# Optimization experiments

Measured on AMD Instinct MI355X. Metric: run time of the kernel, lower is better.

The kernel has to match this reference:

```python
import jax, jax.numpy as jnp
import numpy as np

T, D = 4096, 1536          # tokens, hidden
H, KV, HD = 24, 8, 64      # heads, kv heads, head dim
E, TOPK, F = 32, 8, 512    # experts, top-k, expert intermediate
FS = 1024                  # shared-MLP intermediate
THETA = 10000.0
AMULT = 0.015625           # attention_multiplier (replaces 1/sqrt(hd))
RMULT = 0.22               # residual_multiplier
EPS = 1e-6


def setup_inputs() -> dict:
    key = jax.random.key(0)
    ks = jax.random.split(key, 12)
    s = 0.02
    return {
        'positions': jnp.arange(T, dtype=jnp.int32),
        'hidden_states': jax.random.normal(ks[0], (T, D), jnp.float32),
        'ln1_w': jnp.ones((D,), jnp.float32),
        'wq': jax.random.normal(ks[1], (D, H * HD), jnp.float32) * s,
        'wk': jax.random.normal(ks[2], (D, KV * HD), jnp.float32) * s,
        'wv': jax.random.normal(ks[3], (D, KV * HD), jnp.float32) * s,
        'wo': jax.random.normal(ks[4], (H * HD, D), jnp.float32) * s,
        'ln2_w': jnp.ones((D,), jnp.float32),
        'router_w': jax.random.normal(ks[5], (D, E), jnp.float32) * s,
        'w_gate_up': jax.random.normal(ks[6], (E, D, 2 * F), jnp.float32) * s,
        'w_down': jax.random.normal(ks[7], (E, F, D), jnp.float32) * s,
        'shared_gate_up': jax.random.normal(ks[8], (D, 2 * FS), jnp.float32) * s,
        'shared_down': jax.random.normal(ks[9], (FS, D), jnp.float32) * s,
    }


def _rmsnorm(x, w):
    var = jnp.mean(x * x, axis=-1, keepdims=True)
    return x * jax.lax.rsqrt(var + EPS) * w


def _rope(x, positions):
    # x: [T, nH, HD], neox-style half rotation
    half = HD // 2
    inv_freq = 1.0 / (THETA ** (jnp.arange(half, dtype=jnp.float32) / half))
    ang = positions.astype(jnp.float32)[:, None] * inv_freq[None, :]  # [T, half]
    cos, sin = jnp.cos(ang)[:, None, :], jnp.sin(ang)[:, None, :]
    x1, x2 = x[..., :half], x[..., half:]
    return jnp.concatenate([x1 * cos - x2 * sin, x2 * cos + x1 * sin], axis=-1)


def _silu_and_mul(gu):
    g, u = jnp.split(gu, 2, axis=-1)
    return jax.nn.silu(g) * u


def reference(positions, hidden_states, ln1_w, wq, wk, wv, wo, ln2_w,
              router_w, w_gate_up, w_down, shared_gate_up, shared_down):
    # ---- attention block ----
    residual = hidden_states
    h = _rmsnorm(hidden_states, ln1_w)
    q = _rope((h @ wq).reshape(T, H, HD), positions)
    k = _rope((h @ wk).reshape(T, KV, HD), positions)
    v = (h @ wv).reshape(T, KV, HD)
    k = jnp.repeat(k, H // KV, axis=1)  # GQA expand -> [T, H, HD]
    v = jnp.repeat(v, H // KV, axis=1)
    scores = jnp.einsum('thd,shd->hts', q, k) * AMULT
    mask = jnp.tril(jnp.ones((T, T), dtype=bool))
    scores = jnp.where(mask[None], scores, jnp.finfo(scores.dtype).min)
    probs = jax.nn.softmax(scores, axis=-1)
    attn = jnp.einsum('hts,shd->thd', probs, v).reshape(T, H * HD) @ wo
    hidden = residual + attn * RMULT

    # ---- MoE + shared MLP block ----
    residual = hidden
    h = _rmsnorm(hidden, ln2_w)
    # router: top-k logits, softmax over selected (renormalized gates)
    logits = h @ router_w                          # [T, E]
    topv, topi = jax.lax.top_k(logits, TOPK)       # [T, TOPK]
    gates = jax.nn.softmax(topv, axis=-1)
    # per-token dense expert weight map [T, E] (zero for unselected experts)
    wmap = jnp.sum(jax.nn.one_hot(topi, E, dtype=h.dtype) * gates[..., None], axis=1)
    gu = jnp.einsum('td,edf->tef', h, w_gate_up)   # [T, E, 2F]
    act = _silu_and_mul(gu)                        # [T, E, F]
    moe_out = jnp.einsum('tef,efd,te->td', act, w_down, wmap)
    # shared SiLU MLP
    shared = _silu_and_mul(h @ shared_gate_up) @ shared_down
    hidden = residual + (moe_out + shared) * RMULT
    return hidden
```

## Files before the change

kernel.cpp:

```cpp
#include <hip/hip_runtime.h>
#include <hip/hip_bf16.h>
#include <stdint.h>

using u16 = unsigned short;
using u32 = unsigned int;

typedef __attribute__((ext_vector_type(8))) short short8;
typedef __attribute__((ext_vector_type(4))) short short4v;
typedef __attribute__((ext_vector_type(4))) float f32x4;

#define MFMA16(a,b,c) __builtin_amdgcn_mfma_f32_16x16x32_bf16(a,b,c,0,0,0)
#define QSCL 0.022542110325192448f


__device__ __forceinline__ u16 f2bf(float f){
  __hip_bfloat16 b = __float2bfloat16(f);
  return *reinterpret_cast<u16*>(&b);
}
__device__ __forceinline__ float bf2f(u16 b){ return __uint_as_float(((u32)b)<<16); }

__device__ __forceinline__ void gload16(const void* g, void* l){
  __builtin_amdgcn_global_load_lds(
      (const __attribute__((address_space(1))) u32*)g,
      (__attribute__((address_space(3))) u32*)l, 16, 0, 0);
}

template<int CTRL>
__device__ __forceinline__ float dppf(float x){
  return __int_as_float(__builtin_amdgcn_mov_dpp(__float_as_int(x), CTRL, 0xf, 0xf, true));
}
__device__ __forceinline__ float red16_sum(float x){
  x += dppf<0x128>(x);
  x += dppf<0x124>(x);
  x += dppf<0x122>(x);
  x += dppf<0x121>(x);
  return x;
}

__global__ __launch_bounds__(256) void k_wt(const float* __restrict__ src,
    u16* __restrict__ dst, int K, int N, long sstride, long dstride)
{
  __shared__ float tile[64][65];
  int nb = blockIdx.x*64, kb = blockIdx.y*64;
  const float* S = src + (long)blockIdx.z*sstride;
  u16* D = dst + (long)blockIdx.z*dstride;
  int tid = threadIdx.x;
  int rr = tid>>4, c4 = (tid&15)*4;
  #pragma unroll
  for (int p=0;p<4;++p){
    int r = p*16 + rr;
    f32x4 v = *(const f32x4*)&S[(long)(kb+r)*N + nb + c4];
    tile[r][c4+0]=v[0]; tile[r][c4+1]=v[1]; tile[r][c4+2]=v[2]; tile[r][c4+3]=v[3];
  }
  __syncthreads();
  #pragma unroll
  for (int p=0;p<4;++p){
    int nn = p*16 + rr;
    short4v o;
    #pragma unroll
    for (int i=0;i<4;++i) o[i] = (short)f2bf(tile[c4+i][nn]);
    *(short4v*)&D[(long)(nb+nn)*K + kb + c4] = o;
  }
}

__global__ __launch_bounds__(256) void k_wti(const float* __restrict__ src,
    u16* __restrict__ dst, int K, int N, int halfN, long sstride, long dstride)
{
  __shared__ float tile[64][65];
  int nb = blockIdx.x*64, kb = blockIdx.y*64;
  const float* S = src + (long)blockIdx.z*sstride;
  u16* D = dst + (long)blockIdx.z*dstride;
  int tid = threadIdx.x;
  int rr = tid>>4, c4 = (tid&15)*4;
  int scol = (nb>>1) + ((c4>>5)<<4) + (c4&15) + (((c4>>4)&1)? halfN : 0);
  #pragma unroll
  for (int p=0;p<4;++p){
    int r = p*16 + rr;
    f32x4 v = *(const f32x4*)&S[(long)(kb+r)*N + scol];
    tile[r][c4+0]=v[0]; tile[r][c4+1]=v[1]; tile[r][c4+2]=v[2]; tile[r][c4+3]=v[3];
  }
  __syncthreads();
  #pragma unroll
  for (int p=0;p<4;++p){
    int nn = p*16 + rr;
    short4v o;
    #pragma unroll
    for (int i=0;i<4;++i) o[i] = (short)f2bf(tile[c4+i][nn]);
    *(short4v*)&D[(long)(nb+nn)*K + kb + c4] = o;
  }
}

__global__ __launch_bounds__(256) void k_vt(const u16* __restrict__ v,
                                            u16* __restrict__ vT)
{
  __shared__ u16 t_[64*72];
  int t0 = blockIdx.x*64, kvh = blockIdx.y;
  int tid = threadIdx.x;
  #pragma unroll
  for (int i=0;i<2;++i){
    int c = tid + i*256;
    int row = c>>3, dc = (c&7)*8;
    *(short8*)&t_[row*72 + dc] = *(const short8*)&v[(long)(t0+row)*2560 + kvh*64 + dc];
  }
  __syncthreads();
  #pragma unroll
  for (int i=0;i<2;++i){
    int c = tid + i*256;
    int d = c>>3, tc = (c&7)*8;
    short8 o;
    #pragma unroll
    for (int j=0;j<8;++j) o[j] = (short)t_[(tc+j)*72 + d];
    *(short8*)&vT[(long)(kvh*64 + d)*4096 + t0 + tc] = o;
  }
}

__global__ __launch_bounds__(192) void k_rmsnorm(const float* __restrict__ x,
                                                 const float* __restrict__ w,
                                                 u16* __restrict__ o)
{
  int t = blockIdx.x, tid = threadIdx.x;
  const float* xr = x + (size_t)t*1536 + tid*8;
  f32x4 a = *(const f32x4*)xr;
  f32x4 b = *(const f32x4*)(xr+4);
  float ss = a[0]*a[0]+a[1]*a[1]+a[2]*a[2]+a[3]*a[3]
           + b[0]*b[0]+b[1]*b[1]+b[2]*b[2]+b[3]*b[3];
  #pragma unroll
  for (int m=1;m<64;m<<=1) ss += __shfl_xor(ss,m);
  __shared__ float red[3];
  if ((tid&63)==0) red[tid>>6]=ss;
  __syncthreads();
  float inv = rsqrtf((red[0]+red[1]+red[2])*(1.0f/1536.0f)+1e-6f);
  const float* wp = w + tid*8;
  f32x4 wa = *(const f32x4*)wp;
  f32x4 wb = *(const f32x4*)(wp+4);
  u16* op = o + (size_t)t*1536 + tid*8;
  #pragma unroll
  for (int j=0;j<4;++j) op[j]   = f2bf(a[j]*inv*wa[j]);
  #pragma unroll
  for (int j=0;j<4;++j) op[j+4] = f2bf(b[j]*inv*wb[j]);
}

template<int MODE, int GATHER, int SWZN=0>
__global__ __launch_bounds__(256, (MODE==5||MODE==6)?4:3) void k_gemm(
    const u16* __restrict__ A, int lda,
    const u16* __restrict__ Bt, long strideB, int K,
    int Mfix, const int* __restrict__ cnts, const int* __restrict__ offs,
    const int* __restrict__ toks, const float* __restrict__ gates,
    u16* __restrict__ Cb, int ldcb,
    float* __restrict__ Cf, int ldcf,
    const float* __restrict__ resid, const int* __restrict__ pos)
{
  int e, bx, by;
  if constexpr(SWZN > 0){
    int t = blockIdx.x;
    int elo = t & 7;
    int u = t >> 3;
    int per = SWZN*32;
    int chunk = u / per;
    int inner = u - chunk*per;
    e  = elo + 8*chunk;
    bx = inner % SWZN;
    by = inner / SWZN;
  } else {
    e = blockIdx.z; bx = blockIdx.x; by = blockIdx.y;
  }
  int M = cnts ? cnts[e] : Mfix;
  int m0 = by*128;
  if (m0 >= M) return;
  int roff = offs ? offs[e] : 0;
  const u16* Bp = Bt + (long)e*strideB;
  int col0 = bx*128;

  __shared__ u16 Ash[128*64];
  __shared__ u16 Bsh[128*64];

  int tid = threadIdx.x, wv = tid>>6, lane = tid&63;
  int lr = lane&15, lg = lane>>4;
  int wr = (wv>>1)*64, wc = (wv&1)*64;

  int rsub = lane>>3;
  int ksw = ((lane&7) ^ rsub)*8;
  const u16* apt[4];
  const u16* bpt[4];
  #pragma unroll
  for (int p=0;p<4;++p){
    int rloc = p*32 + wv*8 + rsub;
    int gr = min(m0 + rloc, M-1);
    int ar = GATHER ? toks[roff + gr] : (roff + gr);
    apt[p] = A + (long)ar*lda + ksw;
    bpt[p] = Bp + (long)(col0 + rloc)*K + ksw;
  }

  f32x4 acc[4][4];
  #pragma unroll
  for (int m=0;m<4;++m)
    #pragma unroll
    for (int n=0;n<4;++n)
      acc[m][n] = (f32x4){0.f,0.f,0.f,0.f};

  int nk = K>>6;
  for (int kt=0; kt<nk; ++kt){
    __syncthreads();
    #pragma unroll
    for (int p=0;p<4;++p){
      gload16(apt[p], &Ash[(p*32 + wv*8)*64]);
      gload16(bpt[p], &Bsh[(p*32 + wv*8)*64]);
      apt[p] += 64; bpt[p] += 64;
    }
    __syncthreads();

    #pragma unroll
    for (int kk=0;kk<2;++kk){
      short8 af[4], b1[4];
      #pragma unroll
      for (int m=0;m<4;++m)
        af[m] = *(const short8*)&Ash[(wr+m*16+lr)*64 + (((kk*4+lg)^(lr&7))*8)];
      #pragma unroll
      for (int n=0;n<4;++n)
        b1[n] = *(const short8*)&Bsh[(wc+n*16+lr)*64 + (((kk*4+lg)^(lr&7))*8)];
      #pragma unroll
      for (int m=0;m<4;++m)
        #pragma unroll
        for (int n=0;n<4;++n)
          acc[m][n] = MFMA16(af[m], b1[n], acc[m][n]);
    }
  }

  if constexpr(MODE==6){
    #pragma unroll
    for (int m=0;m<4;++m)
      #pragma unroll
      for (int np=0;np<2;++np)
        #pragma unroll
        for (int rr=0;rr<4;++rr){
          int row = wr + m*16 + lg*4 + rr;
          int gr = m0 + row;
          if (gr >= M) continue;
          float g = acc[m][2*np][rr];
          float u = acc[m][2*np+1][rr];
          float s = g/(1.f+__expf(-g))*u;
          int j = (wc>>1) + np*16 + lr;
          Cb[(long)(roff+gr)*ldcb + (col0>>1) + j] = f2bf(s);
        }
  } else if constexpr(MODE==7){
    if (col0 < 2048){
      float invf0 = __expf(-(float)lr      * 0.28782313662425574f);
      float invf1 = __expf(-(float)(lr+16) * 0.28782313662425574f);
      float qs = (col0 < 1536) ? QSCL : 1.0f;
      #pragma unroll
      for (int m=0;m<4;++m)
        #pragma unroll
        for (int rr=0;rr<4;++rr){
          int gr = m0 + wr + m*16 + lg*4 + rr;
          float pv = (float)pos[gr];
          #pragma unroll
          for (int n=0;n<2;++n){
            float sn, cs;
            __sincosf(pv * (n ? invf1 : invf0), &sn, &cs);
            float x1 = acc[m][n][rr], x2 = acc[m][n+2][rr];
            long base = (long)gr*ldcb + col0 + wc + n*16 + lr;
            Cb[base]      = f2bf((x1*cs - x2*sn)*qs);
            Cb[base + 32] = f2bf((x2*cs + x1*sn)*qs);
          }
        }
    } else {
      #pragma unroll
      for (int m=0;m<4;++m)
        #pragma unroll
        for (int n=0;n<4;++n)
          #pragma unroll
          for (int rr=0;rr<4;++rr){
            int gr = m0 + wr + m*16 + lg*4 + rr;
            int col = wc + n*16 + lr;
            Cb[(long)gr*ldcb + col0 + col] = f2bf(acc[m][n][rr]);
          }
    }
  } else {
    #pragma unroll
    for (int m=0;m<4;++m)
      #pragma unroll
      for (int n=0;n<4;++n)
        #pragma unroll
        for (int rr=0;rr<4;++rr){
          int row = wr + m*16 + lg*4 + rr;
          int gr = m0 + row;
          if (gr >= M) continue;
          int col = wc + n*16 + lr;
          float va = acc[m][n][rr];
          if constexpr(MODE==0){
            Cb[(long)(roff+gr)*ldcb + col0 + col] = f2bf(va);
          } else if constexpr(MODE==1){
            long idx = (long)gr*ldcf + col0 + col;
            Cf[idx] = resid[idx] + va*0.22f;
          } else if constexpr(MODE==5){
            float gt = gates[roff+gr];
            Cb[(long)(roff+gr)*ldcb + col0 + col] = f2bf(va*gt);
          }
        }
  }
}

__global__ __launch_bounds__(192) void k_moesum(const u16* __restrict__ part,
    const int* __restrict__ inv, float* __restrict__ out)
{
  int t = blockIdx.x, tid = threadIdx.x;
  int c = tid*8;
  float s[8] = {0.f,0.f,0.f,0.f,0.f,0.f,0.f,0.f};
  #pragma unroll
  for (int kk=0;kk<8;++kk){
    int slot = inv[t*8+kk];
    short8 v = *(const short8*)&part[(long)slot*1536 + c];
    #pragma unroll
    for (int j=0;j<8;++j) s[j] += bf2f((u16)v[j]);
  }
  float* op = out + (long)t*1536 + c;
  f32x4 o0 = *(const f32x4*)op;
  f32x4 o1 = *(const f32x4*)(op+4);
  #pragma unroll
  for (int j=0;j<4;++j){ o0[j] += s[j]; o1[j] += s[j+4]; }
  *(f32x4*)op = o0;
  *(f32x4*)(op+4) = o1;
}

__global__ __launch_bounds__(256,3) void k_attn(const u16* __restrict__ qg,
    const u16* __restrict__ kg, const u16* __restrict__ vT,
    u16* __restrict__ og, u16* __restrict__ Opart, float* __restrict__ mlb)
{
  int bid = blockIdx.x;
  int kvh = bid & 7;
  int ii = bid >> 3;
  int qt, kt0, kt1, chunk; bool single;
  if (ii < 32)      { qt = 32+ii;        chunk = 0; kt0 = 0;  kt1 = 32;   single = false; }
  else if (ii < 64) { qt = ii;           chunk = 1; kt0 = 32; kt1 = qt+1; single = false; }
  else              { qt = 31-(ii-64);   chunk = 0; kt0 = 0;  kt1 = qt+1; single = true;  }

  int tid = threadIdx.x, wv = tid>>6, lane = tid&63;
  int lr = lane&15, lg = lane>>4;
  __shared__ u16 Ksh[64*72];
  __shared__ u16 Vsh[64*72];
  __shared__ u16 Psh[4][16*68];
  int q0 = qt*64;
  int qrow = q0 + wv*16 + lr;
  short8 qf[3][2];
  #pragma unroll
  for (int hh=0;hh<3;++hh)
    #pragma unroll
    for (int c=0;c<2;++c)
      qf[hh][c] = *(const short8*)&qg[(long)qrow*2560 + (kvh*3+hh)*64 + c*32 + lg*8];

  float l_[3][4];
  f32x4 Ot[3][4];
  #pragma unroll
  for (int hh=0;hh<3;++hh)
    #pragma unroll
    for (int r=0;r<4;++r) l_[hh][r]=0.f;
  #pragma unroll
  for (int hh=0;hh<3;++hh)
    #pragma unroll
    for (int d=0;d<4;++d) Ot[hh][d]=(f32x4){0.f,0.f,0.f,0.f};

  int srow = tid>>3, sdc = (tid&7)*8;
  short8 kreg[2], vreg[2];
  auto loadKV = [&](int kt){
    #pragma unroll
    for (int i=0;i<2;++i){
      int row = srow + i*32;
      kreg[i] = *(const short8*)&kg[(long)(kt*64+row)*2560 + kvh*64 + sdc];
      vreg[i] = *(const short8*)&vT[(long)(kvh*64 + row)*4096 + kt*64 + sdc];
    }
  };
  loadKV(kt0);

  for (int kt=kt0; kt<kt1; ++kt){
    __syncthreads();
    #pragma unroll
    for (int i=0;i<2;++i){
      int row = srow + i*32;
      *(short8*)&Ksh[row*72 + sdc] = kreg[i];
      *(short8*)&Vsh[row*72 + sdc] = vreg[i];
    }
    __syncthreads();
    if (kt < kt1-1) loadKV(kt+1);
    bool diag = (kt==qt);

    #pragma unroll
    for (int hh=0;hh<3;++hh){
      f32x4 S[4];
      #pragma unroll
      for (int n=0;n<4;++n) S[n]=(f32x4){0.f,0.f,0.f,0.f};
      #pragma unroll
      for (int n=0;n<4;++n)
        #pragma unroll
        for (int c=0;c<2;++c){
          short8 kf = *(const short8*)&Ksh[(n*16+lr)*72 + c*32 + lg*8];
          S[n] = MFMA16(qf[hh][c], kf, S[n]);
        }

      float rsum[4] = {0.f,0.f,0.f,0.f};
      #pragma unroll
      for (int n=0;n<4;++n)
        #pragma unroll
        for (int r=0;r<4;++r){
          float sv = S[n][r];
          if (diag){
            int colg = n*16 + lr;
            int rowg = wv*16 + lg*4 + r;
            if (colg > rowg) sv = -1e30f;
          }
          float pv = exp2f(sv);
          S[n][r] = pv;
          rsum[r] += pv;
        }
      #pragma unroll
      for (int r=0;r<4;++r) rsum[r] = red16_sum(rsum[r]);
      #pragma unroll
      for (int r=0;r<4;++r) l_[hh][r] += rsum[r];

      #pragma unroll
      for (int n=0;n<4;++n)
        #pragma unroll
        for (int r=0;r<4;++r)
          Psh[wv][(lg*4+r)*68 + n*16 + lr] = f2bf(S[n][r]);
      #pragma unroll
      for (int c=0;c<2;++c){
        short8 pf = *(const short8*)&Psh[wv][lr*68 + c*32 + lg*8];
        #pragma unroll
        for (int d=0;d<4;++d){
          short8 vf = *(const short8*)&Vsh[(d*16+lr)*72 + c*32 + lg*8];
          Ot[hh][d] = MFMA16(pf, vf, Ot[hh][d]);
        }
      }
    }
  }

  if (single){
    #pragma unroll
    for (int hh=0;hh<3;++hh)
      #pragma unroll
      for (int d=0;d<4;++d)
        #pragma unroll
        for (int r=0;r<4;++r){
          int t = q0 + wv*16 + lg*4 + r;
          og[(long)t*1536 + (kvh*3+hh)*64 + d*16 + lr] = f2bf(Ot[hh][d][r]/l_[hh][r]);
        }
  } else {
    #pragma unroll
    for (int hh=0;hh<3;++hh){
      int h = kvh*3+hh;
      #pragma unroll
      for (int r=0;r<4;++r){
        int t = q0 + wv*16 + lg*4 + r;
        long slot = ((long)(t-2048)*24 + h)*2 + chunk;
        #pragma unroll
        for (int d=0;d<4;++d)
          Opart[slot*64 + d*16 + lr] = f2bf(Ot[hh][d][r]);
        if (lr==0) mlb[slot] = l_[hh][r];
      }
    }
  }
}

__global__ __launch_bounds__(256) void k_comb(const u16* __restrict__ Opart,
    const float* __restrict__ mlb, u16* __restrict__ og)
{
  int gid = blockIdx.x*256 + threadIdx.x;
  int d = gid & 63;
  long rowi = gid >> 6;
  long s0 = rowi*2, s1 = s0+1;
  float l0 = mlb[s0], l1 = mlb[s1];
  float o = (bf2f(Opart[s0*64+d]) + bf2f(Opart[s1*64+d])) / (l0 + l1);
  int t = 2048 + (int)(rowi/24), h = (int)(rowi - (rowi/24)*24);
  og[(long)t*1536 + h*64 + d] = f2bf(o);
}

__global__ __launch_bounds__(256) void k_router(const u16* __restrict__ h2,
    const float* __restrict__ rw, int* __restrict__ topi, float* __restrict__ gatev)
{
  int t = blockIdx.x, tid = threadIdx.x;
  int e = tid & 31, seg = tid >> 5;
  const u16* hr = h2 + (size_t)t*1536 + seg*192;
  const float* wp = rw + (long)seg*192*32 + e;
  float s = 0.f;
  #pragma unroll 4
  for (int d=0; d<192; ++d)
    s += bf2f(hr[d]) * wp[(long)d*32];
  __shared__ float red[8][32];
  red[seg][e] = s;
  __syncthreads();
  __shared__ float lgt[32];
  if (tid < 32){
    float a = 0.f;
    #pragma unroll
    for (int g=0; g<8; ++g) a += red[g][tid];
    lgt[tid] = a;
  }
  __syncthreads();
  if (tid==0){
    u32 msk=0; float tv[8]; int ti[8];
    for (int kk=0;kk<8;++kk){
      float best=-1e30f; int bi=0;
      for (int j2=0;j2<32;++j2)
        if (!((msk>>j2)&1u) && lgt[j2] > best){ best=lgt[j2]; bi=j2; }
      msk |= 1u<<bi; tv[kk]=best; ti[kk]=bi;
    }
    float mx = tv[0], ssum = 0.f, ge[8];
    for (int kk=0;kk<8;++kk){ ge[kk]=__expf(tv[kk]-mx); ssum+=ge[kk]; }
    float isum = 1.f/ssum;
    for (int kk=0;kk<8;++kk){ topi[t*8+kk]=ti[kk]; gatev[t*8+kk]=ge[kk]*isum; }
  }
}

__global__ void k_hist(const int* __restrict__ topi, int* __restrict__ cnt){
  int i = blockIdx.x*256 + threadIdx.x;
  if (i < 4096*8) atomicAdd(&cnt[topi[i]], 1);
}
__global__ void k_scan(const int* __restrict__ cnt, int* __restrict__ offs, int* __restrict__ cur){
  if (threadIdx.x==0 && blockIdx.x==0){
    int a=0;
    for (int e2=0;e2<32;++e2){ offs[e2]=a; cur[e2]=a; a+=cnt[e2]; }
  }
}
__global__ void k_scatter(const int* __restrict__ topi, const float* __restrict__ gatev,
    int* __restrict__ cur, int* __restrict__ toks, float* __restrict__ gts,
    int* __restrict__ inv){
  int i = blockIdx.x*256 + threadIdx.x;
  if (i < 4096*8){
    int e2 = topi[i];
    int p = atomicAdd(&cur[e2], 1);
    toks[p] = i>>3;
    gts[p] = gatev[i]*0.22f;
    inv[i] = p;
  }
}

extern "C" void kernel_launch(void* const* d_in, const int* in_sizes, int n_in,
                              void* d_out, int out_size, void* d_ws, size_t ws_size,
                              hipStream_t stream)
{
  const int*   positions = (const int*)  d_in[0];
  const float* hs   = (const float*)d_in[1];
  const float* ln1w = (const float*)d_in[2];
  const float* wq   = (const float*)d_in[3];
  const float* wk   = (const float*)d_in[4];
  const float* wv   = (const float*)d_in[5];
  const float* wo   = (const float*)d_in[6];
  const float* ln2w = (const float*)d_in[7];
  const float* rww  = (const float*)d_in[8];
  const float* wgu  = (const float*)d_in[9];
  const float* wdn  = (const float*)d_in[10];
  const float* sgu  = (const float*)d_in[11];
  const float* sdn  = (const float*)d_in[12];
  float* out = (float*)d_out;

  char* ws = (char*)d_ws;
  size_t off = 0;
  auto alloc = [&](size_t b)->void*{ void* p = ws + off; off += (b + 255) & ~(size_t)255; return p; };

  u16* hbf     = (u16*)alloc((size_t)4096*1536*2);
  u16* qkv     = (u16*)alloc((size_t)33554432);
  u16* qkvb = qkv;
  u16* aout = qkv + (size_t)4096*2560;
  u16* act_moe = qkv;
  u16* act_sh  = (u16*)alloc((size_t)4096*1024*2);
  u16* vT      = (u16*)alloc((size_t)8*64*4096*2);
  int*   topi  = (int*)  alloc(4096*8*4);
  float* gatev = (float*)alloc(4096*8*4);
  int*   toks  = (int*)  alloc(4096*8*4);
  float* gts   = (float*)alloc(4096*8*4);
  int*   inv   = (int*)  alloc(4096*8*4);
  int*   cnt   = (int*)  alloc(512);
  int*   offs  = (int*)  alloc(512);
  int*   cur   = (int*)  alloc(512);
  u16* wqkvT = (u16*)alloc((size_t)2560*1536*2);
  u16* woT  = (u16*)alloc((size_t)1536*1536*2);
  u16* sguT = (u16*)alloc((size_t)2048*1536*2);
  u16* sdnT = (u16*)alloc((size_t)1536*1024*2);
  u16* wguT = (u16*)alloc((size_t)32*1024*1536*2);
  u16* wdnT = (u16*)alloc((size_t)32*1536*512*2);
  float* hidden2 = out;
  u16*   h2bf = hbf;
  u16*   Opart = hbf;
  float* mlb   = (float*)act_sh;
  u16*   part  = wguT;

  k_wt <<<dim3(24,24,1), 256,0,stream>>>(wq,  wqkvT,                   1536,1536, 0,0);
  k_wt <<<dim3(8,24,1),  256,0,stream>>>(wk,  wqkvT+(size_t)1536*1536, 1536,512,  0,0);
  k_wt <<<dim3(8,24,1),  256,0,stream>>>(wv,  wqkvT+(size_t)2048*1536, 1536,512,  0,0);
  k_wt <<<dim3(24,24,1), 256,0,stream>>>(wo,  woT,  1536,1536, 0,0);
  k_wti<<<dim3(32,24,1), 256,0,stream>>>(sgu, sguT, 1536,2048,1024, 0,0);
  k_wt <<<dim3(24,16,1), 256,0,stream>>>(sdn, sdnT, 1024,1536, 0,0);
  k_wti<<<dim3(16,24,32),256,0,stream>>>(wgu, wguT, 1536,1024,512, (long)1536*1024, (long)1536*1024);
  k_wt <<<dim3(24,8,32), 256,0,stream>>>(wdn, wdnT, 512,1536,  (long)512*1536,  (long)512*1536);

  k_rmsnorm<<<4096,192,0,stream>>>(hs, ln1w, hbf);
  k_gemm<7,0><<<dim3(20,32,1),256,0,stream>>>(hbf,1536, wqkvT,0,1536, 4096,nullptr,nullptr,nullptr,nullptr, qkvb,2560, nullptr,0, nullptr, positions);
  k_vt<<<dim3(64,8,1),256,0,stream>>>(qkvb + 2048, vT);
  k_attn<<<dim3(768,1,1),256,0,stream>>>(qkvb, qkvb + 1536, vT, aout, Opart, mlb);
  k_comb<<<12288,256,0,stream>>>(Opart, mlb, aout);
  k_gemm<1,0><<<dim3(12,32,1),256,0,stream>>>(aout,1536, woT,0,1536, 4096,nullptr,nullptr,nullptr,nullptr, nullptr,0, hidden2,1536, hs, nullptr);
  k_rmsnorm<<<4096,192,0,stream>>>(hidden2, ln2w, h2bf);
  k_router<<<4096,256,0,stream>>>(h2bf, rww, topi, gatev);
  hipMemsetAsync(cnt, 0, 32*4, stream);
  k_hist<<<128,256,0,stream>>>(topi, cnt);
  k_scan<<<1,64,0,stream>>>(cnt, offs, cur);
  k_scatter<<<128,256,0,stream>>>(topi, gatev, cur, toks, gts, inv);
  k_gemm<6,1,8><<<dim3(8192,1,1),256,0,stream>>>(h2bf,1536, wguT,(long)1024*1536,1536, 0,cnt,offs,toks,nullptr, act_moe,512, nullptr,0, nullptr, nullptr);
  k_gemm<6,0><<<dim3(16,32,1),256,0,stream>>>(h2bf,1536, sguT,0,1536, 4096,nullptr,nullptr,nullptr,nullptr, act_sh,1024, nullptr,0, nullptr, nullptr);
  k_gemm<1,0><<<dim3(12,32,1),256,0,stream>>>(act_sh,1024, sdnT,0,1024, 4096,nullptr,nullptr,nullptr,nullptr, nullptr,0, out,1536, out, nullptr);
  k_gemm<5,0,12><<<dim3(12288,1,1),256,0,stream>>>(act_moe,512, wdnT,(long)1536*512,512, 0,cnt,offs,nullptr,gts, part,1536, nullptr,0, nullptr, nullptr);
  k_moesum<<<4096,192,0,stream>>>(part, inv, out);

  (void)in_sizes; (void)n_in; (void)out_size; (void)ws_size;
}
```

Before: 859.1 us.

## Compute router logits with MFMA GEMM using split bf16 hi/lo weights

```diff
diff --git a/kernel.cpp b/kernel.cpp
--- a/kernel.cpp
+++ b/kernel.cpp
@@ -88,6 +88,18 @@
     for (int i=0;i<4;++i) o[i] = (short)f2bf(tile[c4+i][nn]);
     *(short4v*)&D[(long)(nb+nn)*K + kb + c4] = o;
   }
+}
+
+__global__ __launch_bounds__(256) void k_rwt(const float* __restrict__ rw,
+    u16* __restrict__ hi, u16* __restrict__ lo)
+{
+  int i = blockIdx.x*256 + threadIdx.x;
+  int e = i / 1536, d = i - e*1536;
+  float v = rw[(long)d*32 + e];
+  u16 h = f2bf(v);
+  float r = v - bf2f(h);
+  hi[(long)e*1536 + d] = h;
+  lo[(long)e*1536 + d] = f2bf(r);
 }
 
 __global__ __launch_bounds__(256) void k_vt(const u16* __restrict__ v,
@@ -292,12 +304,40 @@
           } else if constexpr(MODE==1){
             long idx = (long)gr*ldcf + col0 + col;
             Cf[idx] = resid[idx] + va*0.22f;
+          } else if constexpr(MODE==3){
+            Cf[(long)gr*ldcf + col0 + col] = va;
+          } else if constexpr(MODE==8){
+            Cf[(long)gr*ldcf + col0 + col] += va;
           } else if constexpr(MODE==5){
             float gt = gates[roff+gr];
             Cb[(long)(roff+gr)*ldcb + col0 + col] = f2bf(va*gt);
           }
         }
   }
+}
+
+__global__ __launch_bounds__(256) void k_top8(const float* __restrict__ logits,
+    int* __restrict__ topi, float* __restrict__ gatev)
+{
+  int t = blockIdx.x*256 + threadIdx.x;
+  float lgt[32];
+  #pragma unroll
+  for (int j=0;j<32;++j) lgt[j] = logits[(long)t*128 + j];
+  u32 msk=0; float tv[8]; int ti[8];
+  #pragma unroll
+  for (int kk=0;kk<8;++kk){
+    float best=-1e30f; int bi=0;
+    #pragma unroll
+    for (int j2=0;j2<32;++j2)
+      if (!((msk>>j2)&1u) && lgt[j2] > best){ best=lgt[j2]; bi=j2; }
+    msk |= 1u<<bi; tv[kk]=best; ti[kk]=bi;
+  }
+  float mx = tv[0], ssum = 0.f, ge[8];
+  #pragma unroll
+  for (int kk=0;kk<8;++kk){ ge[kk]=__expf(tv[kk]-mx); ssum+=ge[kk]; }
+  float isum = 1.f/ssum;
+  #pragma unroll
+  for (int kk=0;kk<8;++kk){ topi[t*8+kk]=ti[kk]; gatev[t*8+kk]=ge[kk]*isum; }
 }
 
 __global__ __launch_bounds__(192) void k_moesum(const u16* __restrict__ part,
@@ -471,43 +511,6 @@
   float o = (bf2f(Opart[s0*64+d]) + bf2f(Opart[s1*64+d])) / (l0 + l1);
   int t = 2048 + (int)(rowi/24), h = (int)(rowi - (rowi/24)*24);
   og[(long)t*1536 + h*64 + d] = f2bf(o);
-}
-
-__global__ __launch_bounds__(256) void k_router(const u16* __restrict__ h2,
-    const float* __restrict__ rw, int* __restrict__ topi, float* __restrict__ gatev)
-{
-  int t = blockIdx.x, tid = threadIdx.x;
-  int e = tid & 31, seg = tid >> 5;
-  const u16* hr = h2 + (size_t)t*1536 + seg*192;
-  const float* wp = rw + (long)seg*192*32 + e;
-  float s = 0.f;
-  #pragma unroll 4
-  for (int d=0; d<192; ++d)
-    s += bf2f(hr[d]) * wp[(long)d*32];
-  __shared__ float red[8][32];
-  red[seg][e] = s;
-  __syncthreads();
-  __shared__ float lgt[32];
-  if (tid < 32){
-    float a = 0.f;
-    #pragma unroll
-    for (int g=0; g<8; ++g) a += red[g][tid];
-    lgt[tid] = a;
-  }
-  __syncthreads();
-  if (tid==0){
-    u32 msk=0; float tv[8]; int ti[8];
-    for (int kk=0;kk<8;++kk){
-      float best=-1e30f; int bi=0;
-      for (int j2=0;j2<32;++j2)
-        if (!((msk>>j2)&1u) && lgt[j2] > best){ best=lgt[j2]; bi=j2; }
-      msk |= 1u<<bi; tv[kk]=best; ti[kk]=bi;
-    }
-    float mx = tv[0], ssum = 0.f, ge[8];
-    for (int kk=0;kk<8;++kk){ ge[kk]=__expf(tv[kk]-mx); ssum+=ge[kk]; }
-    float isum = 1.f/ssum;
-    for (int kk=0;kk<8;++kk){ topi[t*8+kk]=ti[kk]; gatev[t*8+kk]=ge[kk]*isum; }
-  }
 }
 
 __global__ void k_hist(const int* __restrict__ topi, int* __restrict__ cnt){
@@ -563,6 +566,7 @@
   u16* act_moe = qkv;
   u16* act_sh  = (u16*)alloc((size_t)4096*1024*2);
   u16* vT      = (u16*)alloc((size_t)8*64*4096*2);
+  float* logits= (float*)alloc((size_t)4096*128*4);
   int*   topi  = (int*)  alloc(4096*8*4);
   float* gatev = (float*)alloc(4096*8*4);
   int*   toks  = (int*)  alloc(4096*8*4);
@@ -575,6 +579,8 @@
   u16* woT  = (u16*)alloc((size_t)1536*1536*2);
   u16* sguT = (u16*)alloc((size_t)2048*1536*2);
   u16* sdnT = (u16*)alloc((size_t)1536*1024*2);
+  u16* rwhi = (u16*)alloc((size_t)128*1536*2);
+  u16* rwlo = (u16*)alloc((size_t)128*1536*2);
   u16* wguT = (u16*)alloc((size_t)32*1024*1536*2);
   u16* wdnT = (u16*)alloc((size_t)32*1536*512*2);
   float* hidden2 = out;
@@ -591,6 +597,9 @@
   k_wt <<<dim3(24,16,1), 256,0,stream>>>(sdn, sdnT, 1024,1536, 0,0);
   k_wti<<<dim3(16,24,32),256,0,stream>>>(wgu, wguT, 1536,1024,512, (long)1536*1024, (long)1536*1024);
   k_wt <<<dim3(24,8,32), 256,0,stream>>>(wdn, wdnT, 512,1536,  (long)512*1536,  (long)512*1536);
+  hipMemsetAsync(rwhi, 0, (size_t)128*1536*2, stream);
+  hipMemsetAsync(rwlo, 0, (size_t)128*1536*2, stream);
+  k_rwt<<<192,256,0,stream>>>(rww, rwhi, rwlo);
 
   k_rmsnorm<<<4096,192,0,stream>>>(hs, ln1w, hbf);
   k_gemm<7,0><<<dim3(20,32,1),256,0,stream>>>(hbf,1536, wqkvT,0,1536, 4096,nullptr,nullptr,nullptr,nullptr, qkvb,2560, nullptr,0, nullptr, positions);
@@ -599,7 +608,9 @@
   k_comb<<<12288,256,0,stream>>>(Opart, mlb, aout);
   k_gemm<1,0><<<dim3(12,32,1),256,0,stream>>>(aout,1536, woT,0,1536, 4096,nullptr,nullptr,nullptr,nullptr, nullptr,0, hidden2,1536, hs, nullptr);
   k_rmsnorm<<<4096,192,0,stream>>>(hidden2, ln2w, h2bf);
-  k_router<<<4096,256,0,stream>>>(h2bf, rww, topi, gatev);
+  k_gemm<3,0><<<dim3(1,32,1),256,0,stream>>>(h2bf,1536, rwhi,0,1536, 4096,nullptr,nullptr,nullptr,nullptr, nullptr,0, logits,128, nullptr, nullptr);
+  k_gemm<8,0><<<dim3(1,32,1),256,0,stream>>>(h2bf,1536, rwlo,0,1536, 4096,nullptr,nullptr,nullptr,nullptr, nullptr,0, logits,128, nullptr, nullptr);
+  k_top8<<<16,256,0,stream>>>(logits, topi, gatev);
   hipMemsetAsync(cnt, 0, 32*4, stream);
   k_hist<<<128,256,0,stream>>>(topi, cnt);
   k_scan<<<1,64,0,stream>>>(cnt, offs, cur);
```

After: 874.2 us. Within noise of the previous version (+1.8%).
